# Kernel optimization log

Measured on AMD Instinct MI355X. Metric: run time of the kernel, lower is better.

Reference implementation:

```python
import jax, jax.numpy as jnp
import numpy as np

SIZE = 1024
D = 65536


def setup_inputs() -> dict:
    key = jax.random.key(0)
    k_x, k_w, k_b, k_a, k_m = jax.random.split(key, 5)
    x = jax.random.normal(k_x, (SIZE,), dtype=jnp.float32)
    # Projection_2 weight: final init is normal_(0, 1) (normalization in reset_parameters is overwritten)
    weight = jax.random.normal(k_w, (D, SIZE), dtype=jnp.float32)
    # bias ~ Uniform(0, 2*pi), shape (d, size)
    bias = jax.random.uniform(k_b, (D, SIZE), dtype=jnp.float32, minval=0.0, maxval=2.0 * np.pi)
    # alpha[ts] ~ Uniform(0, 1), shape (1, size)
    alpha = jax.random.uniform(k_a, (1, SIZE), dtype=jnp.float32)
    # M is model state (zeros at init, updated online); use random state for a meaningful baseline
    M = jax.random.normal(k_m, (D,), dtype=jnp.float32)
    return {"x": x, "weight": weight, "bias": bias, "alpha": alpha, "M": M, "ts": 0}


def reference(x, weight, bias, alpha, M, ts):
    # ts selects alpha[ts]; alpha is passed directly here.
    # Projection: (1, size) * (d, size) broadcast -> (d, size)
    proj = x[None, :] * weight
    # Nonlinear encode: cos(proj + bias) * sin(proj)
    enc = jnp.cos(proj + bias) * jnp.sin(proj)            # (d, size)
    enc2 = enc * alpha                                     # (d, size)
    # multiset(transpose(enc2)): sum over the size axis -> (d,)
    bundled = enc2.sum(axis=1)
    # hard_quantize: sign to {-1, +1}
    q = jnp.where(bundled > 0, 1.0, -1.0).astype(jnp.float32)  # (d,)
    hvs = enc.T                                            # (size, d)
    # model_result = F.linear(q, M) -> scalar dot product
    model_result = jnp.dot(q, M)
    return (model_result, q, hvs)
```

## Files before the change

### kernel.cpp

```cpp
#include <hip/hip_runtime.h>

#define SIZE_N 1024
#define DDIM   65536
#define D_TILE 64
#define S_CHUNK 64
#define NCHUNK (SIZE_N / S_CHUNK)
#define PITCH  65

__global__ __launch_bounds__(256, 4) void reghd_main(
    const float* __restrict__ x,
    const float* __restrict__ w,
    const float* __restrict__ bias,
    const float* __restrict__ alpha,
    const float* __restrict__ M,
    float* __restrict__ out)
{
    __shared__ float tile[S_CHUNK * PITCH];

    const int t      = threadIdx.x;
    const int lane16 = t & 15;
    const int grp    = t >> 4;
    const int d0     = blockIdx.x * D_TILE;

    float* __restrict__ hvs = out + 1 + DDIM;

    float acc[4] = {0.f, 0.f, 0.f, 0.f};

    for (int c = 0; c < NCHUNK; ++c) {
        const int s0 = c * S_CHUNK;
        const int sx = lane16 * 4;

        const float4 x4 = *reinterpret_cast<const float4*>(x + s0 + sx);
        const float4 a4 = *reinterpret_cast<const float4*>(alpha + s0 + sx);

        #pragma unroll
        for (int p = 0; p < 4; ++p) {
            const int row = grp + 16 * p;
            const size_t base = (size_t)(d0 + row) * SIZE_N + s0 + sx;
            const float4 w4 = *reinterpret_cast<const float4*>(w + base);
            const float4 b4 = *reinterpret_cast<const float4*>(bias + base);

            const float p0 = x4.x * w4.x;
            const float p1 = x4.y * w4.y;
            const float p2 = x4.z * w4.z;
            const float p3 = x4.w * w4.w;
            const float e0 = cosf(p0 + b4.x) * sinf(p0);
            const float e1 = cosf(p1 + b4.y) * sinf(p1);
            const float e2 = cosf(p2 + b4.z) * sinf(p2);
            const float e3 = cosf(p3 + b4.w) * sinf(p3);

            tile[(sx + 0) * PITCH + row] = e0;
            tile[(sx + 1) * PITCH + row] = e1;
            tile[(sx + 2) * PITCH + row] = e2;
            tile[(sx + 3) * PITCH + row] = e3;

            acc[p] += e0 * a4.x + e1 * a4.y + e2 * a4.z + e3 * a4.w;
        }
        __syncthreads();

        #pragma unroll
        for (int p2 = 0; p2 < 16; ++p2) {
            const int idx  = t + 256 * p2;
            const int srow = idx >> 6;
            const int dl   = idx & 63;
            const float v  = tile[srow * PITCH + dl];
            hvs[(size_t)(s0 + srow) * DDIM + d0 + dl] = v;
        }
        __syncthreads();
    }

    float local_dot = 0.f;
    #pragma unroll
    for (int p = 0; p < 4; ++p) {
        float s = acc[p];
        #pragma unroll
        for (int m = 1; m < 16; m <<= 1) s += __shfl_xor(s, m);
        if (lane16 == 0) {
            const int d = d0 + grp + 16 * p;
            const float qv = (s > 0.f) ? 1.f : -1.f;
            out[1 + d] = qv;
            local_dot += qv * M[d];
        }
    }
    local_dot += __shfl_xor(local_dot, 16);
    local_dot += __shfl_xor(local_dot, 32);
    if ((t & 63) == 0) atomicAdd(out, local_dot);
}

extern "C" void kernel_launch(void* const* d_in, const int* in_sizes, int n_in,
                              void* d_out, int out_size, void* d_ws, size_t ws_size,
                              hipStream_t stream) {
    const float* x     = (const float*)d_in[0];
    const float* w     = (const float*)d_in[1];
    const float* bias  = (const float*)d_in[2];
    const float* alpha = (const float*)d_in[3];
    const float* M     = (const float*)d_in[4];
    float* out = (float*)d_out;

    hipMemsetAsync(out, 0, sizeof(float), stream);

    reghd_main<<<dim3(DDIM / D_TILE), dim3(256), 0, stream>>>(x, w, bias, alpha, M, out);
}
```

Before: 731.5 us.

## Double-buffer LDS tile, prefetch next chunk, use nontemporal stores for hvs

Uses two shared-memory tiles so only one barrier per chunk is needed. The weight and bias loads for the next chunk are issued before the current chunk's trig math, so global latency overlaps with compute. The transposed hvs writes now use nontemporal stores and a simpler address stride, and the barrier only waits on LDS counters so outstanding global stores are not drained. This raises register use (prefetched float4s) and doubles LDS, which may reduce occupancy.

Measured after the change: 753.5 us. +3.0%, slower.

```diff
diff --git a/kernel.cpp b/kernel.cpp
--- a/kernel.cpp
+++ b/kernel.cpp
@@ -15,58 +15,84 @@
     const float* __restrict__ M,
     float* __restrict__ out)
 {
-    __shared__ float tile[S_CHUNK * PITCH];
+    __shared__ float tile[2][S_CHUNK * PITCH];
 
     const int t      = threadIdx.x;
     const int lane16 = t & 15;
     const int grp    = t >> 4;
     const int d0     = blockIdx.x * D_TILE;
+    const int sx     = lane16 * 4;
 
     float* __restrict__ hvs = out + 1 + DDIM;
 
+    const int srow0 = t >> 6;
+    const int dl    = t & 63;
+
     float acc[4] = {0.f, 0.f, 0.f, 0.f};
 
+    float4 x4 = *reinterpret_cast<const float4*>(x + sx);
+    float4 a4 = *reinterpret_cast<const float4*>(alpha + sx);
+    float4 w4[4], b4[4];
+    #pragma unroll
+    for (int p = 0; p < 4; ++p) {
+        const size_t base = (size_t)(d0 + grp + 16 * p) * SIZE_N + sx;
+        w4[p] = *reinterpret_cast<const float4*>(w + base);
+        b4[p] = *reinterpret_cast<const float4*>(bias + base);
+    }
+
+    #pragma unroll 2
     for (int c = 0; c < NCHUNK; ++c) {
         const int s0 = c * S_CHUNK;
-        const int sx = lane16 * 4;
+        float* __restrict__ buf = tile[c & 1];
 
-        const float4 x4 = *reinterpret_cast<const float4*>(x + s0 + sx);
-        const float4 a4 = *reinterpret_cast<const float4*>(alpha + s0 + sx);
+        const int s1 = (c + 1 < NCHUNK) ? (s0 + S_CHUNK) : s0;
+        float4 x4n = *reinterpret_cast<const float4*>(x + s1 + sx);
+        float4 a4n = *reinterpret_cast<const float4*>(alpha + s1 + sx);
+        float4 w4n[4], b4n[4];
+        #pragma unroll
+        for (int p = 0; p < 4; ++p) {
+            const size_t base = (size_t)(d0 + grp + 16 * p) * SIZE_N + s1 + sx;
+            w4n[p] = *reinterpret_cast<const float4*>(w + base);
+            b4n[p] = *reinterpret_cast<const float4*>(bias + base);
+        }
 
         #pragma unroll
         for (int p = 0; p < 4; ++p) {
             const int row = grp + 16 * p;
-            const size_t base = (size_t)(d0 + row) * SIZE_N + s0 + sx;
-            const float4 w4 = *reinterpret_cast<const float4*>(w + base);
-            const float4 b4 = *reinterpret_cast<const float4*>(bias + base);
+            const float p0 = x4.x * w4[p].x;
+            const float p1 = x4.y * w4[p].y;
+            const float p2 = x4.z * w4[p].z;
+            const float p3 = x4.w * w4[p].w;
+            const float e0 = cosf(p0 + b4[p].x) * sinf(p0);
+            const float e1 = cosf(p1 + b4[p].y) * sinf(p1);
+            const float e2 = cosf(p2 + b4[p].z) * sinf(p2);
+            const float e3 = cosf(p3 + b4[p].w) * sinf(p3);
 
-            const float p0 = x4.x * w4.x;
-            const float p1 = x4.y * w4.y;
-            const float p2 = x4.z * w4.z;
-            const float p3 = x4.w * w4.w;
-            const float e0 = cosf(p0 + b4.x) * sinf(p0);
-            const float e1 = cosf(p1 + b4.y) * sinf(p1);
-            const float e2 = cosf(p2 + b4.z) * sinf(p2);
-            const float e3 = cosf(p3 + b4.w) * sinf(p3);
-
-            tile[(sx + 0) * PITCH + row] = e0;
-            tile[(sx + 1) * PITCH + row] = e1;
-            tile[(sx + 2) * PITCH + row] = e2;
-            tile[(sx + 3) * PITCH + row] = e3;
+            buf[(sx + 0) * PITCH + row] = e0;
+            buf[(sx + 1) * PITCH + row] = e1;
+            buf[(sx + 2) * PITCH + row] = e2;
+            buf[(sx + 3) * PITCH + row] = e3;
 
             acc[p] += e0 * a4.x + e1 * a4.y + e2 * a4.z + e3 * a4.w;
         }
-        __syncthreads();
 
+        asm volatile("s_waitcnt lgkmcnt(0)" ::: "memory");
+        __builtin_amdgcn_s_barrier();
+        asm volatile("" ::: "memory");
+
+        {
+            const float* lsrc = buf + srow0 * PITCH + dl;
+            float*       gdst = hvs + (size_t)(s0 + srow0) * DDIM + d0 + dl;
+            #pragma unroll
+            for (int p2 = 0; p2 < 16; ++p2) {
+                __builtin_nontemporal_store(lsrc[p2 * 4 * PITCH], gdst);
+                gdst += (size_t)4 * DDIM;
+            }
+        }
+
+        x4 = x4n; a4 = a4n;
         #pragma unroll
-        for (int p2 = 0; p2 < 16; ++p2) {
-            const int idx  = t + 256 * p2;
-            const int srow = idx >> 6;
-            const int dl   = idx & 63;
-            const float v  = tile[srow * PITCH + dl];
-            hvs[(size_t)(s0 + srow) * DDIM + d0 + dl] = v;
-        }
-        __syncthreads();
+        for (int p = 0; p < 4; ++p) { w4[p] = w4n[p]; b4[p] = b4n[p]; }
     }
 
     float local_dot = 0.f;
```
